# Kernel optimization log

Hardware: AMD Instinct MI355X
Metric: run time of the kernel (lower is better)

The kernel has to match this reference:

```python
import jax, jax.numpy as jnp
import numpy as np

# dims: batch, seq, d_model, heads, d_ff, experts, top-k, vocab, layers
B, S, D, H, F, E, K, V, L = 2, 1024, 768, 12, 3072, 8, 2, 32000, 2
EPS = 1e-6


def setup_inputs() -> dict:
    key = jax.random.key(0)
    ks = jax.random.split(key, 12)
    n = lambda k, shape: jax.random.normal(k, shape, jnp.float32) * 0.02
    return {
        "tokens": jax.random.randint(ks[0], (B, S), 0, V),
        "emb": n(ks[1], (V, D)),            # token embedding, tied lm_head
        "pos_emb": n(ks[2], (S, D)),        # learned positions (use_rope=False)
        "wq": n(ks[3], (L, D, D)), "bq": jnp.zeros((L, D), jnp.float32),
        "wk": n(ks[4], (L, D, D)), "bk": jnp.zeros((L, D), jnp.float32),
        "wv": n(ks[5], (L, D, D)), "bv": jnp.zeros((L, D), jnp.float32),
        "wo": n(ks[6], (L, D, D)), "bo": jnp.zeros((L, D), jnp.float32),
        "ln1": jnp.ones((L, D), jnp.float32),
        "ln2": jnp.ones((L, D), jnp.float32),
        "gate_w": n(ks[7], (L, D, E)), "gate_b": jnp.zeros((L, E), jnp.float32),
        "w1": n(ks[8], (L, E, D, F)), "b1": jnp.zeros((L, E, F), jnp.float32),
        "w2": n(ks[9], (L, E, F, D)), "b2": jnp.zeros((L, E, D), jnp.float32),
        "ln_f": jnp.ones((D,), jnp.float32),
    }


def rmsnorm(x, w):
    return x * jax.lax.rsqrt(jnp.mean(x * x, axis=-1, keepdims=True) + EPS) * w


def attention(h, wq, bq, wk, bk, wv, bv, wo, bo):
    hd = D // H
    q = (h @ wq + bq).reshape(B, S, H, hd)
    k = (h @ wk + bk).reshape(B, S, H, hd)
    v = (h @ wv + bv).reshape(B, S, H, hd)
    scores = jnp.einsum('bqhd,bkhd->bhqk', q, k) / np.float32(np.sqrt(hd))
    causal = jnp.tril(jnp.ones((S, S), bool))  # mask = tril(ones(S,S))
    scores = jnp.where(causal, scores, jnp.float32(-1e9))
    probs = jax.nn.softmax(scores, axis=-1)
    out = jnp.einsum('bhqk,bkhd->bqhd', probs, v).reshape(B, S, D)
    return out @ wo + bo


def moe(h, gw, gb, w1, b1, w2, b2):
    # router: top-k over gate logits, softmax over the k selected logits
    logits = h @ gw + gb                                   # [B,S,E]
    top_vals, top_idx = jax.lax.top_k(logits, K)           # [B,S,K]
    w = jax.nn.softmax(top_vals, axis=-1)
    # combined per-expert weight = sum over capacity slots of mask*weight
    one_hot = jax.nn.one_hot(top_idx, E, dtype=h.dtype)    # [B,S,K,E]
    cw = jnp.einsum('bsk,bske->bse', w, one_hot)           # [B,S,E]
    # original computes EVERY expert's FFN on the full token batch, masks after
    h1 = jax.nn.gelu(jnp.einsum('bsd,edf->bsef', h, w1) + b1, approximate=False)
    eo = jnp.einsum('bsef,efd->bsed', h1, w2) + b2         # [B,S,E,D]
    return jnp.einsum('bsed,bse->bsd', eo, cw)


def reference(tokens, emb, pos_emb, wq, bq, wk, bk, wv, bv, wo, bo,
              ln1, ln2, gate_w, gate_b, w1, b1, w2, b2, ln_f):
    x = emb[tokens] + pos_emb[None, :S]                    # [B,S,D]
    for l in range(L):
        x = x + attention(rmsnorm(x, ln1[l]), wq[l], bq[l], wk[l], bk[l],
                          wv[l], bv[l], wo[l], bo[l])
        x = x + moe(rmsnorm(x, ln2[l]), gate_w[l], gate_b[l],
                    w1[l], b1[l], w2[l], b2[l])
    x = rmsnorm(x, ln_f)
    return x @ emb.T                                       # tied lm_head -> [B,S,V]
```

## Files before the change

### kernel.cpp

```cpp
#include <hip/hip_runtime.h>
#include <math.h>

#define TT 2048
#define BB 2
#define SS 1024
#define DD 768
#define HH 12
#define FF 3072
#define EE 8
#define VV 32000
#define NLAYER 2
#define QBLK 8

typedef __attribute__((ext_vector_type(8))) short bf16x8;
typedef __attribute__((ext_vector_type(4))) float f32x4;

static __device__ __forceinline__ unsigned short f2b(float f) {
  unsigned u = __float_as_uint(f);
  unsigned r = (u + 0x7fffu + ((u >> 16) & 1u)) >> 16;
  return (unsigned short)r;
}
static __device__ __forceinline__ unsigned int pk2(float a, float b) {
  return (unsigned int)f2b(a) | ((unsigned int)f2b(b) << 16);
}

__global__ __launch_bounds__(256) void k_embed(const int* __restrict__ tok,
    const float* __restrict__ emb, const float* __restrict__ pos,
    float* __restrict__ x) {
  int t = blockIdx.x;
  int s = t & (SS - 1);
  int tk = tok[t];
  const float* er = emb + (size_t)tk * DD;
  const float* pr = pos + (size_t)s * DD;
  float* xr = x + (size_t)t * DD;
  for (int d = threadIdx.x; d < DD; d += 256)
    xr[d] = er[d] + pr[d];
}

__global__ __launch_bounds__(256) void k_rmsnorm(const float* __restrict__ x,
    const float* __restrict__ w, float* __restrict__ out,
    unsigned short* __restrict__ outb) {
  int t = blockIdx.x;
  const float* xr = x + (size_t)t * DD;
  int tid = threadIdx.x;
  float v0 = xr[tid], v1 = xr[tid + 256], v2 = xr[tid + 512];
  float ss = v0 * v0 + v1 * v1 + v2 * v2;
  for (int off = 32; off > 0; off >>= 1) ss += __shfl_down(ss, off, 64);
  __shared__ float ps[4];
  int wid = tid >> 6, lane = tid & 63;
  if (lane == 0) ps[wid] = ss;
  __syncthreads();
  float r = rsqrtf((ps[0] + ps[1] + ps[2] + ps[3]) * (1.0f / DD) + 1e-6f);
  float* orow = out + (size_t)t * DD;
  unsigned short* brow = outb + (size_t)t * DD;
  float o0 = v0 * r * w[tid], o1 = v1 * r * w[tid + 256], o2 = v2 * r * w[tid + 512];
  orow[tid] = o0; orow[tid + 256] = o1; orow[tid + 512] = o2;
  brow[tid] = f2b(o0); brow[tid + 256] = f2b(o1); brow[tid + 512] = f2b(o2);
}

__global__ __launch_bounds__(256) void k_tcvt(const float* __restrict__ src,
    unsigned short* __restrict__ dst, int R, int C, size_t srcZ, size_t dstZ) {
  src += (size_t)blockIdx.z * srcZ;
  dst += (size_t)blockIdx.z * dstZ;
  __shared__ unsigned short tile[32][40];
  int t = threadIdx.x;
  int r = t >> 3, c4 = (t & 7) * 4;
  int r0 = blockIdx.y * 32, c0 = blockIdx.x * 32;
  float4 v = *(const float4*)(src + (size_t)(r0 + r) * C + c0 + c4);
  tile[r][c4 + 0] = f2b(v.x); tile[r][c4 + 1] = f2b(v.y);
  tile[r][c4 + 2] = f2b(v.z); tile[r][c4 + 3] = f2b(v.w);
  __syncthreads();
  int cc = t >> 3, r4 = (t & 7) * 4;
  ushort4 o;
  o.x = tile[r4 + 0][cc]; o.y = tile[r4 + 1][cc];
  o.z = tile[r4 + 2][cc]; o.w = tile[r4 + 3][cc];
  *(ushort4*)(dst + (size_t)(c0 + cc) * R + r0 + r4) = o;
}

__global__ __launch_bounds__(256) void k_cvt(const float* __restrict__ src,
    unsigned short* __restrict__ dst) {
  size_t i = ((size_t)blockIdx.x * 256 + threadIdx.x) * 8;
  float4 a = *(const float4*)(src + i);
  float4 b = *(const float4*)(src + i + 4);
  ushort4 o0, o1;
  o0.x = f2b(a.x); o0.y = f2b(a.y); o0.z = f2b(a.z); o0.w = f2b(a.w);
  o1.x = f2b(b.x); o1.y = f2b(b.y); o1.z = f2b(b.z); o1.w = f2b(b.w);
  *(ushort4*)(dst + i) = o0;
  *(ushort4*)(dst + i + 4) = o1;
}

template<bool EXPERT>
__global__ __launch_bounds__(256) void k_skf32(
    const float* __restrict__ A, const float* __restrict__ W0,
    const float* __restrict__ W1, const float* __restrict__ W2,
    float* __restrict__ part, int M, int Ntot, int Nthird, int K, int KC,
    int nsplit, int prows,
    const int* __restrict__ counts, const int* __restrict__ bases) {
  int s, base = 0, cnt = M, sel = 0, n0;
  const float* W;
  if (EXPERT) {
    int z = blockIdx.z;
    s = z % nsplit;
    int e = z / nsplit;
    cnt = counts[e]; base = bases[e];
    W = W0 + (size_t)e * K * Nthird;
    n0 = blockIdx.x * 128;
  } else {
    s = blockIdx.z;
    int tpn = Nthird >> 7;
    sel = blockIdx.x / tpn;
    n0 = (blockIdx.x - sel * tpn) * 128;
    W = sel == 0 ? W0 : sel == 1 ? W1 : W2;
  }
  int m0 = blockIdx.y * 128;
  if (EXPERT && m0 >= cnt) return;
  int kbase = s * KC;

  __shared__ float As[16][132];
  __shared__ float Bs[16][132];
  int tid = threadIdx.x;
  int tx = tid & 15, ty = tid >> 4;
  int ra = tid >> 1, ka0 = (tid & 1) * 8;
  int kb = tid >> 4, nb0 = (tid & 15) * 8;
  bool arow_ok = !EXPERT || (m0 + ra < cnt);
  const float* Arow = A + (size_t)(EXPERT ? (base + m0 + (arow_ok ? ra : 0))
                                          : (m0 + ra)) * K + kbase;
  float acc[8][8] = {};
  for (int k0 = 0; k0 < KC; k0 += 16) {
    float4 av0 = make_float4(0.f, 0.f, 0.f, 0.f), av1 = av0;
    if (arow_ok) {
      av0 = *(const float4*)(Arow + k0 + ka0);
      av1 = *(const float4*)(Arow + k0 + ka0 + 4);
    }
    As[ka0 + 0][ra] = av0.x; As[ka0 + 1][ra] = av0.y;
    As[ka0 + 2][ra] = av0.z; As[ka0 + 3][ra] = av0.w;
    As[ka0 + 4][ra] = av1.x; As[ka0 + 5][ra] = av1.y;
    As[ka0 + 6][ra] = av1.z; As[ka0 + 7][ra] = av1.w;
    const float* Wrow = W + (size_t)(kbase + k0 + kb) * Nthird + n0 + nb0;
    *(float4*)&Bs[kb][nb0] = *(const float4*)(Wrow);
    *(float4*)&Bs[kb][nb0 + 4] = *(const float4*)(Wrow + 4);
    __syncthreads();
#pragma unroll
    for (int kk = 0; kk < 16; kk++) {
      float4 a0 = *(const float4*)&As[kk][ty * 8];
      float4 a1 = *(const float4*)&As[kk][ty * 8 + 4];
      float4 b0 = *(const float4*)&Bs[kk][tx * 8];
      float4 b1 = *(const float4*)&Bs[kk][tx * 8 + 4];
      float a[8] = {a0.x, a0.y, a0.z, a0.w, a1.x, a1.y, a1.z, a1.w};
      float b[8] = {b0.x, b0.y, b0.z, b0.w, b1.x, b1.y, b1.z, b1.w};
#pragma unroll
      for (int i = 0; i < 8; i++) {
#pragma unroll
        for (int j = 0; j < 8; j++) acc[i][j] = fmaf(a[i], b[j], acc[i][j]);
      }
    }
    __syncthreads();
  }
#pragma unroll
  for (int i = 0; i < 8; i++) {
    int m = m0 + ty * 8 + i;
    if (EXPERT && m >= cnt) continue;
    size_t prow = EXPERT ? ((size_t)s * prows + base + m) : ((size_t)s * M + m);
    float* orow = part + prow * Ntot + sel * Nthird;
#pragma unroll
    for (int j = 0; j < 8; j++)
      orow[n0 + tx * 8 + j] = acc[i][j];
  }
}

__global__ __launch_bounds__(256) void k_qkvred(const float* __restrict__ part,
    const float* __restrict__ bq, const float* __restrict__ bk,
    const float* __restrict__ bv, float* __restrict__ qb,
    float* __restrict__ kb, float* __restrict__ vb) {
  int t = blockIdx.x;
  for (int c = threadIdx.x; c < 2304; c += 256) {
    float v = part[(size_t)t * 2304 + c] + part[((size_t)TT + t) * 2304 + c];
    if (c < 768)       qb[(size_t)t * DD + c] = v + bq[c];
    else if (c < 1536) kb[(size_t)t * DD + c - 768] = v + bk[c - 768];
    else               vb[(size_t)t * DD + c - 1536] = v + bv[c - 1536];
  }
}

__global__ __launch_bounds__(256) void k_ored(const float* __restrict__ part,
    const float* __restrict__ bo, float* __restrict__ x) {
  int t = blockIdx.x;
  for (int d = threadIdx.x; d < DD; d += 256) {
    float v = part[(size_t)t * DD + d]
            + part[((size_t)TT + t) * DD + d]
            + part[((size_t)2 * TT + t) * DD + d]
            + part[((size_t)3 * TT + t) * DD + d];
    x[(size_t)t * DD + d] += v + bo[d];
  }
}

__global__ __launch_bounds__(256) void k_e2red(const float* __restrict__ part,
    const int* __restrict__ rows, const int* __restrict__ tidx,
    const float* __restrict__ tw, const float* __restrict__ b2,
    float* __restrict__ x) {
  int t = blockIdx.x;
  int r0 = rows[t * 2], r1 = rows[t * 2 + 1];
  int e0 = tidx[t * 2], e1 = tidx[t * 2 + 1];
  float w0 = tw[t * 2], w1 = tw[t * 2 + 1];
  for (int d = threadIdx.x; d < DD; d += 256) {
    float v0 = part[(size_t)r0 * DD + d]
             + part[((size_t)4096 + r0) * DD + d]
             + part[((size_t)8192 + r0) * DD + d]
             + part[((size_t)12288 + r0) * DD + d] + b2[e0 * DD + d];
    float v1 = part[(size_t)r1 * DD + d]
             + part[((size_t)4096 + r1) * DD + d]
             + part[((size_t)8192 + r1) * DD + d]
             + part[((size_t)12288 + r1) * DD + d] + b2[e1 * DD + d];
    x[(size_t)t * DD + d] += w0 * v0 + w1 * v1;
  }
}

__global__ __launch_bounds__(256) void k_attn(const float* __restrict__ q,
    const float* __restrict__ k, const float* __restrict__ v, float* __restrict__ ao) {
  int b = blockIdx.z, hh = blockIdx.y, q0 = blockIdx.x * QBLK;
  __shared__ float qs[QBLK][64];
  __shared__ float sc[QBLK][SS];
  __shared__ float red[QBLK][8];
  int tid = threadIdx.x;
  const size_t hoff = (size_t)b * SS * DD + (size_t)hh * 64;
  for (int i = tid; i < QBLK * 64; i += 256) {
    int qi = i >> 6, d = i & 63;
    qs[qi][d] = q[hoff + (size_t)(q0 + qi) * DD + d];
  }
  __syncthreads();
  int kmax = q0 + QBLK;
  for (int j = tid; j < kmax; j += 256) {
    const float* kr = k + hoff + (size_t)j * DD;
    float p[QBLK];
#pragma unroll
    for (int qi = 0; qi < QBLK; qi++) p[qi] = 0.f;
#pragma unroll 4
    for (int c = 0; c < 16; c++) {
      float4 kv = *(const float4*)(kr + c * 4);
#pragma unroll
      for (int qi = 0; qi < QBLK; qi++)
        p[qi] += qs[qi][c * 4] * kv.x + qs[qi][c * 4 + 1] * kv.y +
                 qs[qi][c * 4 + 2] * kv.z + qs[qi][c * 4 + 3] * kv.w;
    }
#pragma unroll
    for (int qi = 0; qi < QBLK; qi++)
      sc[qi][j] = (j <= q0 + qi) ? p[qi] * 0.125f : -1e30f;
  }
  __syncthreads();
  int wid = tid >> 6, lane = tid & 63;
#pragma unroll
  for (int qi = 0; qi < QBLK; qi++) {
    float mx = -1e30f;
    for (int j = tid; j < kmax; j += 256) mx = fmaxf(mx, sc[qi][j]);
    for (int off = 32; off > 0; off >>= 1) mx = fmaxf(mx, __shfl_down(mx, off, 64));
    if (lane == 0) red[qi][wid] = mx;
  }
  __syncthreads();
#pragma unroll
  for (int qi = 0; qi < QBLK; qi++) {
    float mx = fmaxf(fmaxf(red[qi][0], red[qi][1]), fmaxf(red[qi][2], red[qi][3]));
    float s = 0.f;
    for (int j = tid; j < kmax; j += 256) {
      float e = __expf(sc[qi][j] - mx);
      sc[qi][j] = e;
      s += e;
    }
    for (int off = 32; off > 0; off >>= 1) s += __shfl_down(s, off, 64);
    if (lane == 0) red[qi][4 + wid] = s;
  }
  __syncthreads();
  int d = tid & 63, g = tid >> 6;
  for (int qi = g; qi < QBLK; qi += 4) {
    float inv = 1.f / (red[qi][4] + red[qi][5] + red[qi][6] + red[qi][7]);
    float acc = 0.f;
    int jend = q0 + qi + 1;
    const float* vp = v + hoff + d;
    for (int j = 0; j < jend; j++) acc = fmaf(sc[qi][j], vp[(size_t)j * DD], acc);
    ao[hoff + (size_t)(q0 + qi) * DD + d] = acc * inv;
  }
}

__global__ __launch_bounds__(256) void k_gate(const float* __restrict__ h,
    const float* __restrict__ gw, const float* __restrict__ gb,
    float* __restrict__ glog) {
  __shared__ float hr[DD];
  int t = blockIdx.x;
  for (int d = threadIdx.x; d < DD; d += 256) hr[d] = h[(size_t)t * DD + d];
  __syncthreads();
  int e = threadIdx.x >> 5, j = threadIdx.x & 31;
  float s = 0.f;
  for (int d = j; d < DD; d += 32) s += hr[d] * gw[d * EE + e];
  for (int off = 16; off > 0; off >>= 1) s += __shfl_down(s, off, 32);
  if (j == 0) glog[t * EE + e] = s + gb[e];
}

__global__ void k_zero(int* counts, int* cursor) {
  int i = threadIdx.x;
  if (i < EE) { counts[i] = 0; cursor[i] = 0; }
}

__global__ void k_router(const float* __restrict__ glog, int* __restrict__ tidx,
    float* __restrict__ tw, int* __restrict__ counts) {
  int t = blockIdx.x * 256 + threadIdx.x;
  if (t >= TT) return;
  float l[EE];
#pragma unroll
  for (int e = 0; e < EE; e++) l[e] = glog[t * EE + e];
  int i0 = 0; float v0 = l[0];
#pragma unroll
  for (int e = 1; e < EE; e++) if (l[e] > v0) { v0 = l[e]; i0 = e; }
  int i1 = -1; float v1 = -1e30f;
#pragma unroll
  for (int e = 0; e < EE; e++) if (e != i0 && l[e] > v1) { v1 = l[e]; i1 = e; }
  float e1 = __expf(v1 - v0);
  float inv = 1.f / (1.f + e1);
  tw[t * 2] = inv; tw[t * 2 + 1] = e1 * inv;
  tidx[t * 2] = i0; tidx[t * 2 + 1] = i1;
  atomicAdd(&counts[i0], 1);
  atomicAdd(&counts[i1], 1);
}

__global__ void k_scan(const int* __restrict__ counts, int* __restrict__ bases,
                       int* __restrict__ cursor) {
  int b = 0;
  for (int e = 0; e < EE; e++) { bases[e] = b; cursor[e] = b; b += counts[e]; }
}

__global__ void k_assign(const int* __restrict__ tidx, int* __restrict__ cursor,
                         int* __restrict__ rows, int* __restrict__ gtok) {
  int t = blockIdx.x * 256 + threadIdx.x;
  if (t >= TT) return;
#pragma unroll
  for (int kk = 0; kk < 2; kk++) {
    int e = tidx[t * 2 + kk];
    int r = atomicAdd(&cursor[e], 1);
    rows[t * 2 + kk] = r;
    gtok[r] = t;
  }
}

__global__ __launch_bounds__(256) void k_expert1(const float* __restrict__ h,
    const float* __restrict__ w1, const float* __restrict__ b1,
    const int* __restrict__ gtok, const int* __restrict__ counts,
    const int* __restrict__ bases, float* __restrict__ gh1) {
  int e = blockIdx.z;
  int cnt = counts[e];
  int m0 = blockIdx.y * 128;
  if (m0 >= cnt) return;
  int base = bases[e];
  int n0 = blockIdx.x * 128;
  const float* W = w1 + (size_t)e * DD * FF;
  __shared__ float As[16][132];
  __shared__ float Bs[16][132];
  int tid = threadIdx.x;
  int tx = tid & 15, ty = tid >> 4;
  int ra = tid >> 1, ka0 = (tid & 1) * 8;
  int kb = tid >> 4, nb0 = (tid & 15) * 8;
  int tok = (m0 + ra < cnt) ? gtok[base + m0 + ra] : -1;
  const float* Arow = h + (size_t)(tok < 0 ? 0 : tok) * DD;
  float acc[8][8] = {};
  for (int k0 = 0; k0 < DD; k0 += 16) {
    float4 av0 = make_float4(0.f, 0.f, 0.f, 0.f), av1 = av0;
    if (tok >= 0) {
      av0 = *(const float4*)(Arow + k0 + ka0);
      av1 = *(const float4*)(Arow + k0 + ka0 + 4);
    }
    As[ka0 + 0][ra] = av0.x; As[ka0 + 1][ra] = av0.y;
    As[ka0 + 2][ra] = av0.z; As[ka0 + 3][ra] = av0.w;
    As[ka0 + 4][ra] = av1.x; As[ka0 + 5][ra] = av1.y;
    As[ka0 + 6][ra] = av1.z; As[ka0 + 7][ra] = av1.w;
    const float* Wrow = W + (size_t)(k0 + kb) * FF + n0 + nb0;
    *(float4*)&Bs[kb][nb0] = *(const float4*)(Wrow);
    *(float4*)&Bs[kb][nb0 + 4] = *(const float4*)(Wrow + 4);
    __syncthreads();
#pragma unroll
    for (int kk = 0; kk < 16; kk++) {
      float4 a0 = *(const float4*)&As[kk][ty * 8];
      float4 a1 = *(const float4*)&As[kk][ty * 8 + 4];
      float4 b0 = *(const float4*)&Bs[kk][tx * 8];
      float4 b1 = *(const float4*)&Bs[kk][tx * 8 + 4];
      float a[8] = {a0.x, a0.y, a0.z, a0.w, a1.x, a1.y, a1.z, a1.w};
      float b[8] = {b0.x, b0.y, b0.z, b0.w, b1.x, b1.y, b1.z, b1.w};
#pragma unroll
      for (int i = 0; i < 8; i++) {
#pragma unroll
        for (int j = 0; j < 8; j++) acc[i][j] = fmaf(a[i], b[j], acc[i][j]);
      }
    }
    __syncthreads();
  }
#pragma unroll
  for (int i = 0; i < 8; i++) {
    int m = m0 + ty * 8 + i;
    if (m >= cnt) continue;
    float* orow = gh1 + (size_t)(base + m) * FF;
#pragma unroll
    for (int j = 0; j < 8; j++) {
      int n = n0 + tx * 8 + j;
      float vv = acc[i][j] + b1[e * FF + n];
      orow[n] = 0.5f * vv * (1.f + erff(vv * 0.70710678118654752f));
    }
  }
}

template<bool EXPERT, bool GATHER, bool BIAS, int EPI, bool BF32>
__global__ __launch_bounds__(256) void k_mfma(
    const unsigned short* __restrict__ A, const void* __restrict__ Bt,
    const float* __restrict__ bias, void* __restrict__ Cv,
    int M, int N, int K,
    const int* __restrict__ gtok, const int* __restrict__ counts,
    const int* __restrict__ bases) {
  int cnt = M, base = 0;
  if (EXPERT) {
    int e = blockIdx.z;
    cnt = counts[e]; base = bases[e];
    if (BIAS) bias += (size_t)e * N;
  }
  int m0 = blockIdx.y * 128;
  if (EXPERT && m0 >= cnt) return;
  int n0 = blockIdx.x * 128;

  __shared__ unsigned short As[128 * 40];
  __shared__ unsigned short Bs[128 * 40];

  int tid = threadIdx.x;
  int srow = tid >> 1;
  int scol = (tid & 1) * 16;

  bool avalid = true;
  const unsigned short* arow;
  if (GATHER) {
    avalid = (m0 + srow) < cnt;
    int tk = avalid ? gtok[base + m0 + srow] : 0;
    arow = A + (size_t)tk * K + scol;
  } else if (EXPERT) {
    avalid = (m0 + srow) < cnt;
    arow = A + (size_t)(base + m0 + (avalid ? srow : 0)) * K + scol;
  } else {
    arow = A + (size_t)(m0 + srow) * K + scol;
  }

  const unsigned short* brow16 = nullptr;
  const float* browf = nullptr;
  if (BF32) {
    browf = (const float*)Bt + (size_t)(n0 + srow) * K + scol;
  } else {
    const unsigned short* B16 = (const unsigned short*)Bt;
    if (EXPERT) B16 += (size_t)blockIdx.z * N * K;
    brow16 = B16 + (size_t)(n0 + srow) * K + scol;
  }

  unsigned short* As_w = As + srow * 40 + scol;
  unsigned short* Bs_w = Bs + srow * 40 + scol;

  int lane = tid & 63, wid = tid >> 6;
  int wr = wid >> 1, wc = wid & 1;
  int l15 = lane & 15, lg = lane >> 4;
  const unsigned short* Ar = As + ((wr * 64 + l15) * 40 + lg * 8);
  const unsigned short* Br = Bs + ((wc * 64 + l15) * 40 + lg * 8);

  f32x4 acc[4][4];
#pragma unroll
  for (int i = 0; i < 4; i++)
#pragma unroll
    for (int j = 0; j < 4; j++) acc[i][j] = (f32x4){0.f, 0.f, 0.f, 0.f};

  for (int k0 = 0; k0 < K; k0 += 32) {
    uint4 av0 = {0, 0, 0, 0}, av1 = {0, 0, 0, 0};
    if (avalid) {
      av0 = *(const uint4*)(arow + k0);
      av1 = *(const uint4*)(arow + k0 + 8);
    }
    uint4 bv0, bv1;
    if (BF32) {
      float4 f0 = *(const float4*)(browf + k0);
      float4 f1 = *(const float4*)(browf + k0 + 4);
      float4 f2 = *(const float4*)(browf + k0 + 8);
      float4 f3 = *(const float4*)(browf + k0 + 12);
      bv0 = make_uint4(pk2(f0.x, f0.y), pk2(f0.z, f0.w), pk2(f1.x, f1.y), pk2(f1.z, f1.w));
      bv1 = make_uint4(pk2(f2.x, f2.y), pk2(f2.z, f2.w), pk2(f3.x, f3.y), pk2(f3.z, f3.w));
    } else {
      bv0 = *(const uint4*)(brow16 + k0);
      bv1 = *(const uint4*)(brow16 + k0 + 8);
    }
    *(uint4*)As_w = av0; *(uint4*)(As_w + 8) = av1;
    *(uint4*)Bs_w = bv0; *(uint4*)(Bs_w + 8) = bv1;
    __syncthreads();
    bf16x8 af[4], bfr[4];
#pragma unroll
    for (int f = 0; f < 4; f++) {
      af[f]  = *(const bf16x8*)(Ar + f * 640);
      bfr[f] = *(const bf16x8*)(Br + f * 640);
    }
#pragma unroll
    for (int i = 0; i < 4; i++)
#pragma unroll
      for (int j = 0; j < 4; j++)
        acc[i][j] = __builtin_amdgcn_mfma_f32_16x16x32_bf16(af[i], bfr[j], acc[i][j], 0, 0, 0);
    __syncthreads();
  }

#pragma unroll
  for (int j = 0; j < 4; j++) {
    int n = n0 + wc * 64 + j * 16 + l15;
    float bb = BIAS ? bias[n] : 0.f;
#pragma unroll
    for (int i = 0; i < 4; i++) {
      int mb = m0 + wr * 64 + i * 16 + lg * 4;
#pragma unroll
      for (int r = 0; r < 4; r++) {
        int m = mb + r;
        if (EXPERT && m >= cnt) continue;
        size_t off = (size_t)(base + m) * N + n;
        float v = acc[i][j][r] + bb;
        if (EPI == 0) {
          ((float*)Cv)[off] = v;
        } else {
          float g = 0.5f * v * (1.f + erff(v * 0.70710678118654752f));
          ((unsigned short*)Cv)[off] = f2b(g);
        }
      }
    }
  }
}

__global__ __launch_bounds__(256) void k_scatter(const float* __restrict__ go,
    const int* __restrict__ rows, const float* __restrict__ tw, float* __restrict__ x) {
  int t = blockIdx.x;
  int r0 = rows[t * 2], r1 = rows[t * 2 + 1];
  float w0 = tw[t * 2], w1 = tw[t * 2 + 1];
  float* xr = x + (size_t)t * DD;
  const float* g0 = go + (size_t)r0 * DD;
  const float* g1 = go + (size_t)r1 * DD;
  for (int d = threadIdx.x; d < DD; d += 256)
    xr[d] += w0 * g0[d] + w1 * g1[d];
}

extern "C" void kernel_launch(void* const* d_in, const int* in_sizes, int n_in,
                              void* d_out, int out_size, void* d_ws, size_t ws_size,
                              hipStream_t stream) {
  (void)in_sizes; (void)n_in; (void)out_size;
  const int* tok   = (const int*)d_in[0];
  const float* emb = (const float*)d_in[1];
  const float* pos = (const float*)d_in[2];
  const float* wq  = (const float*)d_in[3];
  const float* bq  = (const float*)d_in[4];
  const float* wk  = (const float*)d_in[5];
  const float* bk  = (const float*)d_in[6];
  const float* wv  = (const float*)d_in[7];
  const float* bvv = (const float*)d_in[8];
  const float* wo  = (const float*)d_in[9];
  const float* bo  = (const float*)d_in[10];
  const float* ln1 = (const float*)d_in[11];
  const float* ln2 = (const float*)d_in[12];
  const float* gw  = (const float*)d_in[13];
  const float* gb  = (const float*)d_in[14];
  const float* w1  = (const float*)d_in[15];
  const float* b1  = (const float*)d_in[16];
  const float* w2  = (const float*)d_in[17];
  const float* b2  = (const float*)d_in[18];
  const float* lnf = (const float*)d_in[19];

  float* fp = (float*)d_out;
  float* qb   = fp; fp += (size_t)TT * DD;
  float* kb   = fp; fp += (size_t)TT * DD;
  float* vb   = fp; fp += (size_t)TT * DD;
  float* ao   = fp; fp += (size_t)TT * DD;
  float* x    = fp; fp += (size_t)TT * DD;
  float* h    = fp; fp += (size_t)TT * DD;
  float* gh1  = fp; fp += (size_t)TT * 2 * FF;
  float* go   = fp; fp += (size_t)TT * 2 * DD;
  float* glog = fp; fp += (size_t)TT * EE;
  float* tw   = fp; fp += (size_t)TT * 2;
  int* tidx   = (int*)fp; fp += TT * 2;
  int* rows   = (int*)fp; fp += TT * 2;
  int* gtok   = (int*)fp; fp += TT * 2;
  int* counts = (int*)fp; fp += 16;
  int* cursor = (int*)fp; fp += 16;
  int* bases  = (int*)fp; fp += 16;
  unsigned short* hb   = (unsigned short*)fp; fp += (size_t)TT * DD / 2;
  unsigned short* gh1b = (unsigned short*)fp; fp += (size_t)TT * 2 * FF / 2;
  unsigned short* w1t  = (unsigned short*)fp; fp += (size_t)EE * DD * FF / 2;
  unsigned short* w2t  = (unsigned short*)fp; fp += (size_t)EE * FF * DD / 2;
  float* part = fp; fp += (size_t)4 * 4096 * DD;

  unsigned short* hf = (unsigned short*)d_ws;
  unsigned short* embT = (unsigned short*)d_ws + (size_t)TT * DD;
  bool useEmbT = ws_size >= (size_t)TT * DD * 2 + (size_t)VV * DD * 2;

  k_embed<<<TT, 256, 0, stream>>>(tok, emb, pos, x);
  k_tcvt<<<dim3(96, 24, EE), 256, 0, stream>>>(w1 + (size_t)1 * EE * DD * FF, w1t,
      DD, FF, (size_t)DD * FF, (size_t)DD * FF);
  k_tcvt<<<dim3(24, 96, EE), 256, 0, stream>>>(w2 + (size_t)1 * EE * FF * DD, w2t,
      FF, DD, (size_t)FF * DD, (size_t)FF * DD);
  if (useEmbT)
    k_cvt<<<(VV * DD) / (256 * 8), 256, 0, stream>>>(emb, embT);

  for (int l = 0; l < NLAYER; l++) {
    const float* wq_l = wq + (size_t)l * DD * DD;
    const float* wk_l = wk + (size_t)l * DD * DD;
    const float* wv_l = wv + (size_t)l * DD * DD;
    const float* wo_l = wo + (size_t)l * DD * DD;

    k_rmsnorm<<<TT, 256, 0, stream>>>(x, ln1 + (size_t)l * DD, h, hb);
    k_skf32<false><<<dim3(18, 16, 2), 256, 0, stream>>>(h, wq_l, wk_l, wv_l,
        part, TT, 2304, 768, 768, 384, 2, TT, nullptr, nullptr);
    k_qkvred<<<TT, 256, 0, stream>>>(part, bq + (size_t)l * DD, bk + (size_t)l * DD,
        bvv + (size_t)l * DD, qb, kb, vb);
    k_attn<<<dim3(SS / QBLK, HH, BB), 256, 0, stream>>>(qb, kb, vb, ao);
    k_skf32<false><<<dim3(6, 16, 4), 256, 0, stream>>>(ao, wo_l, wo_l, wo_l,
        part, TT, 768, 768, 768, 192, 4, TT, nullptr, nullptr);
    k_ored<<<TT, 256, 0, stream>>>(part, bo + (size_t)l * DD, x);

    k_rmsnorm<<<TT, 256, 0, stream>>>(x, ln2 + (size_t)l * DD, h, hb);
    k_gate<<<TT, 256, 0, stream>>>(h, gw + (size_t)l * DD * EE, gb + (size_t)l * EE, glog);
    k_zero<<<1, 64, 0, stream>>>(counts, cursor);
    k_router<<<TT / 256, 256, 0, stream>>>(glog, tidx, tw, counts);
    k_scan<<<1, 1, 0, stream>>>(counts, bases, cursor);
    k_assign<<<TT / 256, 256, 0, stream>>>(tidx, cursor, rows, gtok);
    if (l < NLAYER - 1) {
      k_expert1<<<dim3(FF / 128, TT / 128, EE), 256, 0, stream>>>(
          h, w1 + (size_t)l * EE * DD * FF, b1 + (size_t)l * EE * FF,
          gtok, counts, bases, gh1);
      k_skf32<true><<<dim3(6, 16, 32), 256, 0, stream>>>(gh1,
          w2 + (size_t)l * EE * FF * DD, nullptr, nullptr,
          part, TT, 768, 768, FF, 768, 4, 4096, counts, bases);
      k_e2red<<<TT, 256, 0, stream>>>(part, rows, tidx, tw,
          b2 + (size_t)l * EE * DD, x);
    } else {
      k_mfma<true, true, true, 2, false><<<dim3(FF / 128, TT / 128, EE), 256, 0, stream>>>(
          hb, w1t, b1 + (size_t)l * EE * FF, gh1b,
          TT, FF, DD, gtok, counts, bases);
      k_mfma<true, false, true, 0, false><<<dim3(DD / 128, TT / 128, EE), 256, 0, stream>>>(
          gh1b, w2t, b2 + (size_t)l * EE * DD, go,
          TT, DD, FF, gtok, counts, bases);
      k_scatter<<<TT, 256, 0, stream>>>(go, rows, tw, x);
    }
  }

  k_rmsnorm<<<TT, 256, 0, stream>>>(x, lnf, h, hf);
  if (useEmbT) {
    k_mfma<false, false, false, 0, false><<<dim3(VV / 128, TT / 128), 256, 0, stream>>>(
        hf, embT, nullptr, (float*)d_out,
        TT, VV, DD, nullptr, nullptr, nullptr);
  } else {
    k_mfma<false, false, false, 0, true><<<dim3(VV / 128, TT / 128), 256, 0, stream>>>(
        hf, emb, nullptr, (float*)d_out,
        TT, VV, DD, nullptr, nullptr, nullptr);
  }
}
```

Baseline: 2.274 ms.

## Read GEMM weights directly, swizzle expert B tile, split attention PV accumulators

The generic split-K GEMM drops its shared-memory B tile and has each thread load its 8 weight columns straight from global memory in the inner k loop. The expert1 kernel swizzles the float4 column index of its B shared tile to reduce LDS bank conflicts. The attention PV loop is unrolled by four with independent accumulators to shorten the FMA dependency chain. Direct global reads of B give up the reuse that shared memory provided across the 16 row-groups and rely on cache hits, and the reordered accumulation changes floating-point summation order slightly.

```diff
diff --git a/kernel.cpp b/kernel.cpp
--- a/kernel.cpp
+++ b/kernel.cpp
@@ -117,14 +117,13 @@
   int kbase = s * KC;
 
   __shared__ float As[16][132];
-  __shared__ float Bs[16][132];
   int tid = threadIdx.x;
   int tx = tid & 15, ty = tid >> 4;
   int ra = tid >> 1, ka0 = (tid & 1) * 8;
-  int kb = tid >> 4, nb0 = (tid & 15) * 8;
   bool arow_ok = !EXPERT || (m0 + ra < cnt);
   const float* Arow = A + (size_t)(EXPERT ? (base + m0 + (arow_ok ? ra : 0))
                                           : (m0 + ra)) * K + kbase;
+  const float* Wp = W + (size_t)kbase * Nthird + n0 + tx * 8;
   float acc[8][8] = {};
   for (int k0 = 0; k0 < KC; k0 += 16) {
     float4 av0 = make_float4(0.f, 0.f, 0.f, 0.f), av1 = av0;
@@ -136,16 +135,14 @@
     As[ka0 + 2][ra] = av0.z; As[ka0 + 3][ra] = av0.w;
     As[ka0 + 4][ra] = av1.x; As[ka0 + 5][ra] = av1.y;
     As[ka0 + 6][ra] = av1.z; As[ka0 + 7][ra] = av1.w;
-    const float* Wrow = W + (size_t)(kbase + k0 + kb) * Nthird + n0 + nb0;
-    *(float4*)&Bs[kb][nb0] = *(const float4*)(Wrow);
-    *(float4*)&Bs[kb][nb0 + 4] = *(const float4*)(Wrow + 4);
     __syncthreads();
+    const float* Wk = Wp;
 #pragma unroll
     for (int kk = 0; kk < 16; kk++) {
+      float4 b0 = *(const float4*)(Wk);
+      float4 b1 = *(const float4*)(Wk + 4);
       float4 a0 = *(const float4*)&As[kk][ty * 8];
       float4 a1 = *(const float4*)&As[kk][ty * 8 + 4];
-      float4 b0 = *(const float4*)&Bs[kk][tx * 8];
-      float4 b1 = *(const float4*)&Bs[kk][tx * 8 + 4];
       float a[8] = {a0.x, a0.y, a0.z, a0.w, a1.x, a1.y, a1.z, a1.w};
       float b[8] = {b0.x, b0.y, b0.z, b0.w, b1.x, b1.y, b1.z, b1.w};
 #pragma unroll
@@ -153,7 +150,9 @@
 #pragma unroll
         for (int j = 0; j < 8; j++) acc[i][j] = fmaf(a[i], b[j], acc[i][j]);
       }
-    }
+      Wk += Nthird;
+    }
+    Wp += (size_t)Nthird * 16;
     __syncthreads();
   }
 #pragma unroll
@@ -271,10 +270,18 @@
   int d = tid & 63, g = tid >> 6;
   for (int qi = g; qi < QBLK; qi += 4) {
     float inv = 1.f / (red[qi][4] + red[qi][5] + red[qi][6] + red[qi][7]);
-    float acc = 0.f;
     int jend = q0 + qi + 1;
     const float* vp = v + hoff + d;
-    for (int j = 0; j < jend; j++) acc = fmaf(sc[qi][j], vp[(size_t)j * DD], acc);
+    float a0 = 0.f, a1 = 0.f, a2 = 0.f, a3 = 0.f;
+    int j = 0;
+    for (; j + 4 <= jend; j += 4) {
+      a0 = fmaf(sc[qi][j],     vp[(size_t)j * DD], a0);
+      a1 = fmaf(sc[qi][j + 1], vp[(size_t)(j + 1) * DD], a1);
+      a2 = fmaf(sc[qi][j + 2], vp[(size_t)(j + 2) * DD], a2);
+      a3 = fmaf(sc[qi][j + 3], vp[(size_t)(j + 3) * DD], a3);
+    }
+    for (; j < jend; j++) a0 = fmaf(sc[qi][j], vp[(size_t)j * DD], a0);
+    float acc = (a0 + a2) + (a1 + a3);
     ao[hoff + (size_t)(q0 + qi) * DD + d] = acc * inv;
   }
 }
@@ -354,7 +361,10 @@
   int tid = threadIdx.x;
   int tx = tid & 15, ty = tid >> 4;
   int ra = tid >> 1, ka0 = (tid & 1) * 8;
-  int kb = tid >> 4, nb0 = (tid & 15) * 8;
+  int kb = tid >> 4;
+  int g1 = 2 * tx, g2 = 2 * tx + 1;
+  int cw1 = (g1 ^ ((g1 >> 3) & 1)) << 2;
+  int cw2 = (g2 ^ ((g2 >> 3) & 1)) << 2;
   int tok = (m0 + ra < cnt) ? gtok[base + m0 + ra] : -1;
   const float* Arow = h + (size_t)(tok < 0 ? 0 : tok) * DD;
   float acc[8][8] = {};
@@ -368,16 +378,16 @@
     As[ka0 + 2][ra] = av0.z; As[ka0 + 3][ra] = av0.w;
     As[ka0 + 4][ra] = av1.x; As[ka0 + 5][ra] = av1.y;
     As[ka0 + 6][ra] = av1.z; As[ka0 + 7][ra] = av1.w;
-    const float* Wrow = W + (size_t)(k0 + kb) * FF + n0 + nb0;
-    *(float4*)&Bs[kb][nb0] = *(const float4*)(Wrow);
-    *(float4*)&Bs[kb][nb0 + 4] = *(const float4*)(Wrow + 4);
+    const float* Wrow = W + (size_t)(k0 + kb) * FF + n0 + tx * 8;
+    *(float4*)&Bs[kb][cw1] = *(const float4*)(Wrow);
+    *(float4*)&Bs[kb][cw2] = *(const float4*)(Wrow + 4);
     __syncthreads();
 #pragma unroll
     for (int kk = 0; kk < 16; kk++) {
       float4 a0 = *(const float4*)&As[kk][ty * 8];
       float4 a1 = *(const float4*)&As[kk][ty * 8 + 4];
-      float4 b0 = *(const float4*)&Bs[kk][tx * 8];
-      float4 b1 = *(const float4*)&Bs[kk][tx * 8 + 4];
+      float4 b0 = *(const float4*)&Bs[kk][cw1];
+      float4 b1 = *(const float4*)&Bs[kk][cw2];
       float a[8] = {a0.x, a0.y, a0.z, a0.w, a1.x, a1.y, a1.z, a1.w};
       float b[8] = {b0.x, b0.y, b0.z, b0.w, b1.x, b1.y, b1.z, b1.w};
 #pragma unroll
```

After: 2.895 ms. 27.3% more time.
